# Kernel optimization log

Measured on AMD Instinct MI355X. Metric: run time of the kernel, lower is better.

The kernel has to match this reference:

```python
import jax, jax.numpy as jnp
import numpy as np

N_NODES = 50000
N_EDGES = 600000
IN_FEATS = 128
OUT_FEATS = 128


def setup_inputs() -> dict:
    key = jax.random.key(0)
    k1, k2, k3, k4, k5 = jax.random.split(key, 5)
    edge_row = jax.random.randint(k1, (N_EDGES,), 0, N_NODES, dtype=jnp.int32)
    edge_col = jax.random.randint(k2, (N_EDGES,), 0, N_NODES, dtype=jnp.int32)
    edge_vals = jax.random.uniform(k3, (N_EDGES,), dtype=jnp.float32)
    node_embs = jax.random.normal(k4, (N_NODES, IN_FEATS), dtype=jnp.float32)
    gcn_weight = jax.random.normal(k5, (IN_FEATS, OUT_FEATS), dtype=jnp.float32) / np.sqrt(IN_FEATS)
    return {"edge_row": edge_row, "edge_col": edge_col, "edge_vals": edge_vals,
            "node_embs": node_embs, "gcn_weight": gcn_weight}


def reference(edge_row, edge_col, edge_vals, node_embs, gcn_weight):
    # SpMM: Ahat @ node_embs, with Ahat in COO form (row, col, val)
    gathered = node_embs[edge_col] * edge_vals[:, None]          # [E, in_feats]
    agg = jax.ops.segment_sum(gathered, edge_row, num_segments=N_NODES)  # [N, in_feats]
    # dense GEMM + activation
    out = jax.nn.relu(agg @ gcn_weight)                          # [N, out_feats]
    return out
```

## Files before the change

kernel.cpp:

```cpp
#include <hip/hip_runtime.h>
#include <hip/hip_fp16.h>

#define NN 50000
#define NE 600000
#define F  128
#define CAP 128

#define WS_NEEDED 64200064u

#define FMA4(ACC, AS, WV) \
    ACC.x += (AS) * WV.x; ACC.y += (AS) * WV.y; ACC.z += (AS) * WV.z; ACC.w += (AS) * WV.w;

__global__ __launch_bounds__(256) void k_gemm_xw(const float* __restrict__ X,
                                                 const float* __restrict__ W,
                                                 __half* __restrict__ XW,
                                                 int* __restrict__ cnt) {
    {
        int gtid = blockIdx.x * 256 + threadIdx.x;
        if (gtid < NN) cnt[gtid] = 0;
    }

    __shared__ float Wl[64][128];
    __shared__ float Al[64][128];
    const int tid = threadIdx.x;
    const int rg  = tid >> 5;
    const int oq  = (tid & 31) << 2;
    const int row0 = blockIdx.x * 64;

    #pragma unroll
    for (int i = 0; i < 8; ++i) {
        int idx4 = i * 256 + tid;
        int r  = idx4 >> 5;
        int cc = (idx4 & 31) << 2;
        int grow = row0 + r;
        float4 v = make_float4(0.f, 0.f, 0.f, 0.f);
        if (grow < NN)
            v = *reinterpret_cast<const float4*>(X + (size_t)grow * F + cc);
        *reinterpret_cast<float4*>(&Al[r][cc]) = v;
    }

    float4 acc[8];
    #pragma unroll
    for (int j = 0; j < 8; ++j) acc[j] = make_float4(0.f, 0.f, 0.f, 0.f);

    for (int kk = 0; kk < 2; ++kk) {
        if (kk) __syncthreads();
        #pragma unroll
        for (int i = 0; i < 8; ++i) {
            int idx4 = i * 256 + tid;
            *reinterpret_cast<float4*>(reinterpret_cast<float*>(Wl) + idx4 * 4) =
                *reinterpret_cast<const float4*>(W + kk * 64 * F + idx4 * 4);
        }
        __syncthreads();
        #pragma unroll 2
        for (int k4 = 0; k4 < 64; k4 += 4) {
            float4 w0 = *reinterpret_cast<const float4*>(&Wl[k4 + 0][oq]);
            float4 w1 = *reinterpret_cast<const float4*>(&Wl[k4 + 1][oq]);
            float4 w2 = *reinterpret_cast<const float4*>(&Wl[k4 + 2][oq]);
            float4 w3 = *reinterpret_cast<const float4*>(&Wl[k4 + 3][oq]);
            #pragma unroll
            for (int r = 0; r < 8; ++r) {
                float4 a = *reinterpret_cast<const float4*>(&Al[rg * 8 + r][kk * 64 + k4]);
                FMA4(acc[r], a.x, w0)
                FMA4(acc[r], a.y, w1)
                FMA4(acc[r], a.z, w2)
                FMA4(acc[r], a.w, w3)
            }
        }
    }
    #pragma unroll
    for (int r = 0; r < 8; ++r) {
        int grow = row0 + rg * 8 + r;
        if (grow < NN) {
            float4 a = acc[r];
            __half2 lo = __float22half2_rn(make_float2(a.x, a.y));
            __half2 hi = __float22half2_rn(make_float2(a.z, a.w));
            uint2 pk;
            pk.x = *reinterpret_cast<unsigned*>(&lo);
            pk.y = *reinterpret_cast<unsigned*>(&hi);
            *reinterpret_cast<uint2*>(XW + (size_t)grow * F + oq) = pk;
        }
    }
}

__global__ __launch_bounds__(256) void k_fill_bucket(const int4* __restrict__ erow4,
                                                     const int4* __restrict__ ecol4,
                                                     const float4* __restrict__ eval4,
                                                     int* __restrict__ cnt,
                                                     int2* __restrict__ pairs) {
    int t = blockIdx.x * 256 + threadIdx.x;
    if (t * 4 >= NE) return;
    int4   r4 = erow4[t];
    int4   c4 = ecol4[t];
    float4 v4 = eval4[t];
    int p0 = atomicAdd(&cnt[r4.x], 1);
    int p1 = atomicAdd(&cnt[r4.y], 1);
    int p2 = atomicAdd(&cnt[r4.z], 1);
    int p3 = atomicAdd(&cnt[r4.w], 1);
    if (p0 < CAP) pairs[(size_t)r4.x * CAP + p0] = make_int2(c4.x, __float_as_int(v4.x));
    if (p1 < CAP) pairs[(size_t)r4.y * CAP + p1] = make_int2(c4.y, __float_as_int(v4.y));
    if (p2 < CAP) pairs[(size_t)r4.z * CAP + p2] = make_int2(c4.z, __float_as_int(v4.z));
    if (p3 < CAP) pairs[(size_t)r4.w * CAP + p3] = make_int2(c4.w, __float_as_int(v4.w));
}

#define GATH(EIDX, AIDX) { \
    int2 ee = bp[EIDX]; \
    float2 xx = __half22float2(*reinterpret_cast<const __half2*>(Xl + ee.x * F)); \
    float vv = __int_as_float(ee.y); \
    AIDX.x += xx.x * vv; AIDX.y += xx.y * vv; }

__global__ __launch_bounds__(256) void k_agg_relu(const int* __restrict__ cnt,
                                                  const int2* __restrict__ pairs,
                                                  const __half* __restrict__ XW,
                                                  float* __restrict__ out) {
    const int wid  = threadIdx.x >> 6;
    const int lane = threadIdx.x & 63;
    const int node = blockIdx.x * 4 + wid;
    if (node >= NN) return;
    int n = cnt[node];
    n = (n > CAP) ? CAP : n;
    const int2* bp = pairs + (size_t)node * CAP;
    const __half* Xl = XW + lane * 2;
    float2 a0 = make_float2(0.f, 0.f), a1 = a0, a2 = a0, a3 = a0;
    float2 a4 = a0, a5 = a0, a6 = a0, a7 = a0;
    int i = 0;
    for (; i + 8 <= n; i += 8) {
        GATH(i + 0, a0) GATH(i + 1, a1) GATH(i + 2, a2) GATH(i + 3, a3)
        GATH(i + 4, a4) GATH(i + 5, a5) GATH(i + 6, a6) GATH(i + 7, a7)
    }
    if (i + 4 <= n) {
        GATH(i + 0, a0) GATH(i + 1, a1) GATH(i + 2, a2) GATH(i + 3, a3)
        i += 4;
    }
    for (; i < n; ++i) GATH(i, a0)
    float2 r = make_float2(((a0.x + a1.x) + (a2.x + a3.x)) + ((a4.x + a5.x) + (a6.x + a7.x)),
                           ((a0.y + a1.y) + (a2.y + a3.y)) + ((a4.y + a5.y) + (a6.y + a7.y)));
    r.x = fmaxf(r.x, 0.f);
    r.y = fmaxf(r.y, 0.f);
    *reinterpret_cast<float2*>(out + (size_t)node * F + lane * 2) = r;
}

__global__ void k_zero_f4(float4* __restrict__ p, int n4) {
    int i = blockIdx.x * blockDim.x + threadIdx.x;
    if (i < n4) p[i] = make_float4(0.f, 0.f, 0.f, 0.f);
}

__global__ void k_scatter(const int* __restrict__ erow, const int* __restrict__ ecol,
                          const float* __restrict__ eval, const float* __restrict__ X,
                          float* __restrict__ agg) {
    unsigned tid = blockIdx.x * blockDim.x + threadIdx.x;
    unsigned e = tid >> 5;
    if (e >= NE) return;
    unsigned f = (tid & 31u) << 2;
    int   r = erow[e];
    int   c = ecol[e];
    float v = eval[e];
    float4 x = *reinterpret_cast<const float4*>(X + (size_t)c * F + f);
    float* dst = agg + (size_t)r * F + f;
    atomicAdd(dst + 0, x.x * v);
    atomicAdd(dst + 1, x.y * v);
    atomicAdd(dst + 2, x.z * v);
    atomicAdd(dst + 3, x.w * v);
}

__global__ __launch_bounds__(256) void k_gemm_relu(float* __restrict__ io,
                                                   const float* __restrict__ W) {
    __shared__ float Wl[64][128];
    __shared__ float Al[64][128];
    const int tid = threadIdx.x;
    const int rg  = tid >> 5;
    const int oq  = (tid & 31) << 2;
    const int row0 = blockIdx.x * 64;

    #pragma unroll
    for (int i = 0; i < 8; ++i) {
        int idx4 = i * 256 + tid;
        int r  = idx4 >> 5;
        int cc = (idx4 & 31) << 2;
        int grow = row0 + r;
        float4 v = make_float4(0.f, 0.f, 0.f, 0.f);
        if (grow < NN)
            v = *reinterpret_cast<const float4*>(io + (size_t)grow * F + cc);
        *reinterpret_cast<float4*>(&Al[r][cc]) = v;
    }
    float4 acc[8];
    #pragma unroll
    for (int j = 0; j < 8; ++j) acc[j] = make_float4(0.f, 0.f, 0.f, 0.f);
    for (int kk = 0; kk < 2; ++kk) {
        if (kk) __syncthreads();
        #pragma unroll
        for (int i = 0; i < 8; ++i) {
            int idx4 = i * 256 + tid;
            *reinterpret_cast<float4*>(reinterpret_cast<float*>(Wl) + idx4 * 4) =
                *reinterpret_cast<const float4*>(W + kk * 64 * F + idx4 * 4);
        }
        __syncthreads();
        #pragma unroll 2
        for (int k4 = 0; k4 < 64; k4 += 4) {
            float4 w0 = *reinterpret_cast<const float4*>(&Wl[k4 + 0][oq]);
            float4 w1 = *reinterpret_cast<const float4*>(&Wl[k4 + 1][oq]);
            float4 w2 = *reinterpret_cast<const float4*>(&Wl[k4 + 2][oq]);
            float4 w3 = *reinterpret_cast<const float4*>(&Wl[k4 + 3][oq]);
            #pragma unroll
            for (int r = 0; r < 8; ++r) {
                float4 a = *reinterpret_cast<const float4*>(&Al[rg * 8 + r][kk * 64 + k4]);
                FMA4(acc[r], a.x, w0)
                FMA4(acc[r], a.y, w1)
                FMA4(acc[r], a.z, w2)
                FMA4(acc[r], a.w, w3)
            }
        }
    }
    #pragma unroll
    for (int r = 0; r < 8; ++r) {
        int grow = row0 + rg * 8 + r;
        if (grow < NN) {
            float4 a = acc[r];
            a.x = fmaxf(a.x, 0.f);
            a.y = fmaxf(a.y, 0.f);
            a.z = fmaxf(a.z, 0.f);
            a.w = fmaxf(a.w, 0.f);
            *reinterpret_cast<float4*>(io + (size_t)grow * F + oq) = a;
        }
    }
}

extern "C" void kernel_launch(void* const* d_in, const int* in_sizes, int n_in,
                              void* d_out, int out_size, void* d_ws, size_t ws_size,
                              hipStream_t stream) {
    const int*   erow  = (const int*)d_in[0];
    const int*   ecol  = (const int*)d_in[1];
    const float* evals = (const float*)d_in[2];
    const float* X     = (const float*)d_in[3];
    const float* W     = (const float*)d_in[4];
    float* out = (float*)d_out;

    if (ws_size >= WS_NEEDED) {
        char* ws = (char*)d_ws;
        int*    cnt   = (int*)(ws + 0);
        int2*   pairs = (int2*)(ws + 200064);
        __half* XW    = (__half*)(ws + 51400064);

        k_gemm_xw<<<(NN + 63) / 64, 256, 0, stream>>>(X, W, XW, cnt);
        const int ng = NE / 4;
        k_fill_bucket<<<(ng + 255) / 256, 256, 0, stream>>>(
            (const int4*)erow, (const int4*)ecol, (const float4*)evals, cnt, pairs);
        k_agg_relu<<<(NN + 3) / 4, 256, 0, stream>>>(cnt, pairs, XW, out);
    } else {
        const int n4 = NN * F / 4;
        k_zero_f4<<<(n4 + 255) / 256, 256, 0, stream>>>((float4*)out, n4);
        k_scatter<<<(NE * 32) / 256, 256, 0, stream>>>(erow, ecol, evals, X, out);
        k_gemm_relu<<<(NN + 63) / 64, 256, 0, stream>>>(out, W);
    }
}
```

Before: 99.88 us.

## Fuse bucket fill into GEMM launch and split wave across edges in aggregation

```diff
diff --git a/kernel.cpp b/kernel.cpp
--- a/kernel.cpp
+++ b/kernel.cpp
@@ -5,27 +5,50 @@
 #define NE 600000
 #define F  128
 #define CAP 128
+#define NFILL_BLK 586
+#define NGEMM_BLK 782
 
 #define WS_NEEDED 64200064u
+
+__global__ void k_zero4(int4* __restrict__ p, int n4) {
+    int i = blockIdx.x * blockDim.x + threadIdx.x;
+    if (i < n4) p[i] = make_int4(0, 0, 0, 0);
+}
 
 #define FMA4(ACC, AS, WV) \
     ACC.x += (AS) * WV.x; ACC.y += (AS) * WV.y; ACC.z += (AS) * WV.z; ACC.w += (AS) * WV.w;
 
-__global__ __launch_bounds__(256) void k_gemm_xw(const float* __restrict__ X,
-                                                 const float* __restrict__ W,
-                                                 __half* __restrict__ XW,
-                                                 int* __restrict__ cnt) {
-    {
-        int gtid = blockIdx.x * 256 + threadIdx.x;
-        if (gtid < NN) cnt[gtid] = 0;
-    }
-
+__global__ __launch_bounds__(256) void k_gemm_fill(const float* __restrict__ X,
+                                                   const float* __restrict__ W,
+                                                   __half* __restrict__ XW,
+                                                   const int4* __restrict__ erow4,
+                                                   const int4* __restrict__ ecol4,
+                                                   const float4* __restrict__ eval4,
+                                                   int* __restrict__ cnt,
+                                                   int2* __restrict__ pairs) {
+    if (blockIdx.x < NFILL_BLK) {
+        int t = blockIdx.x * 256 + threadIdx.x;
+        if (t * 4 < NE) {
+            int4   r4 = erow4[t];
+            int4   c4 = ecol4[t];
+            float4 v4 = eval4[t];
+            int p0 = atomicAdd(&cnt[r4.x], 1);
+            int p1 = atomicAdd(&cnt[r4.y], 1);
+            int p2 = atomicAdd(&cnt[r4.z], 1);
+            int p3 = atomicAdd(&cnt[r4.w], 1);
+            if (p0 < CAP) pairs[(size_t)r4.x * CAP + p0] = make_int2(c4.x, __float_as_int(v4.x));
+            if (p1 < CAP) pairs[(size_t)r4.y * CAP + p1] = make_int2(c4.y, __float_as_int(v4.y));
+            if (p2 < CAP) pairs[(size_t)r4.z * CAP + p2] = make_int2(c4.z, __float_as_int(v4.z));
+            if (p3 < CAP) pairs[(size_t)r4.w * CAP + p3] = make_int2(c4.w, __float_as_int(v4.w));
+        }
+        return;
+    }
     __shared__ float Wl[64][128];
     __shared__ float Al[64][128];
     const int tid = threadIdx.x;
     const int rg  = tid >> 5;
     const int oq  = (tid & 31) << 2;
-    const int row0 = blockIdx.x * 64;
+    const int row0 = (blockIdx.x - NFILL_BLK) * 64;
 
     #pragma unroll
     for (int i = 0; i < 8; ++i) {
@@ -83,31 +106,13 @@
     }
 }
 
-__global__ __launch_bounds__(256) void k_fill_bucket(const int4* __restrict__ erow4,
-                                                     const int4* __restrict__ ecol4,
-                                                     const float4* __restrict__ eval4,
-                                                     int* __restrict__ cnt,
-                                                     int2* __restrict__ pairs) {
-    int t = blockIdx.x * 256 + threadIdx.x;
-    if (t * 4 >= NE) return;
-    int4   r4 = erow4[t];
-    int4   c4 = ecol4[t];
-    float4 v4 = eval4[t];
-    int p0 = atomicAdd(&cnt[r4.x], 1);
-    int p1 = atomicAdd(&cnt[r4.y], 1);
-    int p2 = atomicAdd(&cnt[r4.z], 1);
-    int p3 = atomicAdd(&cnt[r4.w], 1);
-    if (p0 < CAP) pairs[(size_t)r4.x * CAP + p0] = make_int2(c4.x, __float_as_int(v4.x));
-    if (p1 < CAP) pairs[(size_t)r4.y * CAP + p1] = make_int2(c4.y, __float_as_int(v4.y));
-    if (p2 < CAP) pairs[(size_t)r4.z * CAP + p2] = make_int2(c4.z, __float_as_int(v4.z));
-    if (p3 < CAP) pairs[(size_t)r4.w * CAP + p3] = make_int2(c4.w, __float_as_int(v4.w));
-}
-
-#define GATH(EIDX, AIDX) { \
-    int2 ee = bp[EIDX]; \
-    float2 xx = __half22float2(*reinterpret_cast<const __half2*>(Xl + ee.x * F)); \
-    float vv = __int_as_float(ee.y); \
-    AIDX.x += xx.x * vv; AIDX.y += xx.y * vv; }
+#define PGATH(I, ACC) { \
+    int2 e = bp[(I) + half]; \
+    float v = __int_as_float(e.y); \
+    uint2 h4 = *reinterpret_cast<const uint2*>(XW + (size_t)e.x * F + (li << 2)); \
+    float2 flo = __half22float2(*reinterpret_cast<__half2*>(&h4.x)); \
+    float2 fhi = __half22float2(*reinterpret_cast<__half2*>(&h4.y)); \
+    ACC.x += flo.x * v; ACC.y += flo.y * v; ACC.z += fhi.x * v; ACC.w += fhi.y * v; }
 
 __global__ __launch_bounds__(256) void k_agg_relu(const int* __restrict__ cnt,
                                                   const int2* __restrict__ pairs,
@@ -120,24 +125,40 @@
     int n = cnt[node];
     n = (n > CAP) ? CAP : n;
     const int2* bp = pairs + (size_t)node * CAP;
-    const __half* Xl = XW + lane * 2;
-    float2 a0 = make_float2(0.f, 0.f), a1 = a0, a2 = a0, a3 = a0;
-    float2 a4 = a0, a5 = a0, a6 = a0, a7 = a0;
+    const int half = lane >> 5;
+    const int li   = lane & 31;
+
+    float4 a0 = make_float4(0.f, 0.f, 0.f, 0.f), a1 = a0, a2 = a0, a3 = a0;
     int i = 0;
     for (; i + 8 <= n; i += 8) {
-        GATH(i + 0, a0) GATH(i + 1, a1) GATH(i + 2, a2) GATH(i + 3, a3)
-        GATH(i + 4, a4) GATH(i + 5, a5) GATH(i + 6, a6) GATH(i + 7, a7)
-    }
-    if (i + 4 <= n) {
-        GATH(i + 0, a0) GATH(i + 1, a1) GATH(i + 2, a2) GATH(i + 3, a3)
-        i += 4;
-    }
-    for (; i < n; ++i) GATH(i, a0)
-    float2 r = make_float2(((a0.x + a1.x) + (a2.x + a3.x)) + ((a4.x + a5.x) + (a6.x + a7.x)),
-                           ((a0.y + a1.y) + (a2.y + a3.y)) + ((a4.y + a5.y) + (a6.y + a7.y)));
-    r.x = fmaxf(r.x, 0.f);
-    r.y = fmaxf(r.y, 0.f);
-    *reinterpret_cast<float2*>(out + (size_t)node * F + lane * 2) = r;
+        PGATH(i + 0, a0) PGATH(i + 2, a1) PGATH(i + 4, a2) PGATH(i + 6, a3)
+    }
+    if (i + 4 <= n) { PGATH(i + 0, a0) PGATH(i + 2, a1) i += 4; }
+    if (i + 2 <= n) { PGATH(i + 0, a2) i += 2; }
+    if (i < n) {
+        int2 e = bp[i];
+        float v = (half == 0) ? __int_as_float(e.y) : 0.f;
+        uint2 h4 = *reinterpret_cast<const uint2*>(XW + (size_t)e.x * F + (li << 2));
+        float2 flo = __half22float2(*reinterpret_cast<__half2*>(&h4.x));
+        float2 fhi = __half22float2(*reinterpret_cast<__half2*>(&h4.y));
+        a3.x += flo.x * v; a3.y += flo.y * v; a3.z += fhi.x * v; a3.w += fhi.y * v;
+    }
+    float4 s;
+    s.x = (a0.x + a1.x) + (a2.x + a3.x);
+    s.y = (a0.y + a1.y) + (a2.y + a3.y);
+    s.z = (a0.z + a1.z) + (a2.z + a3.z);
+    s.w = (a0.w + a1.w) + (a2.w + a3.w);
+    s.x += __shfl_xor(s.x, 32);
+    s.y += __shfl_xor(s.y, 32);
+    s.z += __shfl_xor(s.z, 32);
+    s.w += __shfl_xor(s.w, 32);
+    if (half == 0) {
+        s.x = fmaxf(s.x, 0.f);
+        s.y = fmaxf(s.y, 0.f);
+        s.z = fmaxf(s.z, 0.f);
+        s.w = fmaxf(s.w, 0.f);
+        *reinterpret_cast<float4*>(out + (size_t)node * F + (li << 2)) = s;
+    }
 }
 
 __global__ void k_zero_f4(float4* __restrict__ p, int n4) {
@@ -241,10 +262,10 @@
         int2*   pairs = (int2*)(ws + 200064);
         __half* XW    = (__half*)(ws + 51400064);
 
-        k_gemm_xw<<<(NN + 63) / 64, 256, 0, stream>>>(X, W, XW, cnt);
-        const int ng = NE / 4;
-        k_fill_bucket<<<(ng + 255) / 256, 256, 0, stream>>>(
-            (const int4*)erow, (const int4*)ecol, (const float4*)evals, cnt, pairs);
+        k_zero4<<<(NN / 4 + 255) / 256, 256, 0, stream>>>((int4*)cnt, NN / 4);
+        k_gemm_fill<<<NFILL_BLK + NGEMM_BLK, 256, 0, stream>>>(
+            X, W, XW, (const int4*)erow, (const int4*)ecol, (const float4*)evals,
+            cnt, pairs);
         k_agg_relu<<<(NN + 3) / 4, 256, 0, stream>>>(cnt, pairs, XW, out);
     } else {
         const int n4 = NN * F / 4;
```

Result: faster. 95.52 us (-4.4%).
